# Optimization experiments

Measured on AMD Instinct MI355X. Metric: run time of the kernel, lower is better.

Reference implementation:

```python
import jax, jax.numpy as jnp
import numpy as np

N, E, F_IN, H, H2, G, C = 30000, 480000, 1280, 512, 256, 64, 10


def _linear_init(key, fan_in, fan_out):
    k1, k2 = jax.random.split(key)
    s = 1.0 / np.sqrt(fan_in)
    W = jax.random.uniform(k1, (fan_in, fan_out), jnp.float32, -s, s)
    b = jax.random.uniform(k2, (fan_out,), jnp.float32, -s, s)
    return W, b


def setup_inputs() -> dict:
    key = jax.random.key(0)
    ks = jax.random.split(key, 6)
    x = jax.random.normal(ks[0], (N, F_IN), jnp.float32)
    edge_index = jax.random.randint(ks[1], (2, E), 0, N, dtype=jnp.int32).astype(jnp.int64)
    batch = jnp.sort(jax.random.randint(ks[2], (N,), 0, G, dtype=jnp.int32)).astype(jnp.int64)
    W1, b1 = _linear_init(ks[3], F_IN, H)
    beta2 = jnp.ones((), jnp.float32)  # AGNNConv beta init = 1.0 (trainable in prop2)
    W2, b2 = _linear_init(ks[4], H, H2)
    W3, b3 = _linear_init(ks[5], 2 * H2, C)
    return {"x": x, "edge_index": edge_index, "batch": batch,
            "W1": W1, "b1": b1, "beta2": beta2,
            "W2": W2, "b2": b2, "W3": W3, "b3": b3}


def _agnn(x, src, dst, beta, n):
    # L2 normalize (PyG F.normalize: clamp norm at 1e-12)
    norm = jnp.maximum(jnp.linalg.norm(x, axis=-1, keepdims=True), 1e-12)
    xn = x / norm
    # per-edge cosine similarity attention logits
    alpha = beta * jnp.sum(xn[src] * xn[dst], axis=-1)  # [E']
    # softmax over incoming edges of each destination node
    amax = jax.ops.segment_max(alpha, dst, num_segments=n)
    ex = jnp.exp(alpha - amax[dst])
    denom = jax.ops.segment_sum(ex, dst, num_segments=n)
    w = ex / denom[dst]
    # weighted scatter-add of raw source features
    return jax.ops.segment_sum(w[:, None] * x[src], dst, num_segments=n)


def reference(x, edge_index, batch, W1, b1, beta2, W2, b2, W3, b3):
    n = x.shape[0]
    h = jax.nn.relu(x @ W1 + b1)  # [N, 512]
    # AGNNConv adds self-loops by default
    loops = jnp.arange(n, dtype=edge_index.dtype)
    src = jnp.concatenate([edge_index[0], loops])
    dst = jnp.concatenate([edge_index[1], loops])
    h = _agnn(h, src, dst, jnp.float32(1.0), n)  # prop1: fixed beta=1
    h = _agnn(h, src, dst, beta2, n)             # prop2: learned beta
    h = jax.nn.relu(h @ W2 + b2)  # [N, 256]
    # global max / mean pool per graph
    gmx = jax.ops.segment_max(h, batch, num_segments=G)
    cnt = jnp.maximum(jax.ops.segment_sum(jnp.ones((n,), h.dtype), batch, num_segments=G), 1.0)
    gav = jax.ops.segment_sum(h, batch, num_segments=G) / cnt[:, None]
    return jnp.concatenate([gmx, gav], axis=1) @ W3 + b3  # [G, C]
```

## Files before the change

### kernel.cpp

```cpp
#include <hip/hip_runtime.h>
#include <hip/hip_bf16.h>
#include <cstdint>


typedef __attribute__((ext_vector_type(8))) short bf16x8;
typedef __attribute__((ext_vector_type(4))) float f32x4;
typedef __attribute__((ext_vector_type(8))) unsigned short ushort8;
typedef __attribute__((ext_vector_type(4))) unsigned short ushort4v;
typedef __attribute__((ext_vector_type(4))) unsigned int uint4v;

__device__ inline unsigned short f2bf(float f) {
    unsigned int u = __float_as_uint(f);
    u += 0x7FFFu + ((u >> 16) & 1u);
    return (unsigned short)(u >> 16);
}

__device__ __forceinline__ float bf2f(unsigned short u) {
    return __uint_as_float(((unsigned int)u) << 16);
}

__device__ __forceinline__ unsigned int cvtpk(float lo, float hi) {
    unsigned int r;
    asm("v_cvt_pk_bf16_f32 %0, %1, %2" : "=v"(r) : "v"(lo), "v"(hi));
    return r;
}

__device__ __forceinline__ void gload_lds16(const void* g, void* l) {
    __builtin_amdgcn_global_load_lds(
        (const __attribute__((address_space(1))) void*)g,
        (__attribute__((address_space(3))) void*)l, 16, 0, 0);
}

__device__ __forceinline__ float wave_sum_dpp(float p) {
    int t;
    t = __builtin_amdgcn_update_dpp(0, __float_as_int(p), 0xB1, 0xf, 0xf, true);
    p += __int_as_float(t);
    t = __builtin_amdgcn_update_dpp(0, __float_as_int(p), 0x4E, 0xf, 0xf, true);
    p += __int_as_float(t);
    t = __builtin_amdgcn_update_dpp(0, __float_as_int(p), 0x141, 0xf, 0xf, true);
    p += __int_as_float(t);
    t = __builtin_amdgcn_update_dpp(0, __float_as_int(p), 0x140, 0xf, 0xf, true);
    p += __int_as_float(t);
    t = __builtin_amdgcn_update_dpp(0, __float_as_int(p), 0x142, 0xf, 0xf, true);
    p += __int_as_float(t);
    t = __builtin_amdgcn_update_dpp(0, __float_as_int(p), 0x143, 0xf, 0xf, true);
    p += __int_as_float(t);
    return __int_as_float(__builtin_amdgcn_readlane(__float_as_int(p), 63));
}

__device__ __forceinline__ float row16_sum_dpp(float p) {
    int t;
    t = __builtin_amdgcn_update_dpp(0, __float_as_int(p), 0xB1, 0xf, 0xf, true);
    p += __int_as_float(t);
    t = __builtin_amdgcn_update_dpp(0, __float_as_int(p), 0x4E, 0xf, 0xf, true);
    p += __int_as_float(t);
    t = __builtin_amdgcn_update_dpp(0, __float_as_int(p), 0x141, 0xf, 0xf, true);
    p += __int_as_float(t);
    t = __builtin_amdgcn_update_dpp(0, __float_as_int(p), 0x140, 0xf, 0xf, true);
    p += __int_as_float(t);
    return p;
}

__global__ __launch_bounds__(256) void k_transpose_both(
    const float* __restrict__ W1, unsigned short* __restrict__ W1T,
    int K1, int N1, int nt1,
    const float* __restrict__ W2, unsigned short* __restrict__ W2T,
    int K2, int N2) {
    __shared__ unsigned short tb[32][33];
    int id = blockIdx.x;
    const float* W; unsigned short* Wt; int K, N, bx, by;
    if (id < nt1) {
        W = W1; Wt = W1T; K = K1; N = N1;
        int nx = K1 / 32; bx = id % nx; by = id / nx;
    } else {
        id -= nt1;
        W = W2; Wt = W2T; K = K2; N = N2;
        int nx = K2 / 32; bx = id % nx; by = id / nx;
    }
    int k0 = bx * 32, n0 = by * 32;
    int tr = threadIdx.x >> 3;
    int tc = (threadIdx.x & 7) * 4;
    float4 v = *(const float4*)(W + (long)(k0 + tr) * N + n0 + tc);
    tb[tr][tc + 0] = f2bf(v.x); tb[tr][tc + 1] = f2bf(v.y);
    tb[tr][tc + 2] = f2bf(v.z); tb[tr][tc + 3] = f2bf(v.w);
    __syncthreads();
    ushort4v o = { tb[tc + 0][tr], tb[tc + 1][tr], tb[tc + 2][tr], tb[tc + 3][tr] };
    *(ushort4v*)(Wt + (long)(n0 + tr) * K + k0 + tc) = o;
}

template <int K, int BN, int NOUT, bool AF32, bool OUTBF16, bool PSUM_EN>
__global__ __launch_bounds__(512, 4) void k_gemm_bias_relu(
    const void* __restrict__ Av, const unsigned short* __restrict__ Bt,
    const float* __restrict__ bias, void* __restrict__ Cv,
    float* __restrict__ psum, int M) {
    constexpr int NSTEP = K / 32;
    constexpr int NF = BN / 64;
    constexpr int SLOTS = (NOUT / BN) * 4;
    __shared__ unsigned short As[2][128 * 32];
    __shared__ unsigned short Bs[2][BN * 32];
    int tid = threadIdx.x;
    int w = tid >> 6, l = tid & 63;
    int wm = w >> 2, wn = w & 3;
    int mBase = blockIdx.x * 128;
    int nBase = blockIdx.y * BN;

    const float* Af = (const float*)Av;
    const unsigned short* Ab = (const unsigned short*)Av;

    int arow = tid >> 2;
    int aslot = (tid & 3) ^ ((arow >> 1) & 3);
    long aRowG = mBase + arow; if (aRowG >= M) aRowG = M - 1;
    const float* aptr = AF32 ? (Af + aRowG * K + (tid & 3) * 8) : nullptr;

    auto stageB = [&](int b, int k0) {
#pragma unroll
        for (int o = 0; o < (BN + 127) / 128; ++o) {
            int rbase = (w * ((BN + 127) / 128) + o) * 16;
            int row = rbase + (l >> 2);
            int gsrc = (l & 3) ^ ((row >> 1) & 3);
            gload_lds16(Bt + (long)(nBase + row) * K + k0 + gsrc * 8,
                        &Bs[b][rbase * 32]);
        }
    };
    auto stageAbf = [&](int b, int k0) {
        int rbase = w * 16;
        int row = rbase + (l >> 2);
        int gsrc = (l & 3) ^ ((row >> 1) & 3);
        long gr = mBase + row; if (gr >= M) gr = M - 1;
        gload_lds16(Ab + gr * K + k0 + gsrc * 8, &As[b][rbase * 32]);
    };

    f32x4 acc[4][NF] = {};

    stageB(0, 0);
    if constexpr (AF32) {
        float4 z0 = *(const float4*)(aptr);
        float4 z1 = *(const float4*)(aptr + 4);
        uint4v p = { cvtpk(z0.x, z0.y), cvtpk(z0.z, z0.w),
                     cvtpk(z1.x, z1.y), cvtpk(z1.z, z1.w) };
        *(uint4v*)(&As[0][arow * 32 + aslot * 8]) = p;
    } else {
        stageAbf(0, 0);
    }
    __syncthreads();

    int s = 0;
    for (int step = 0; step < NSTEP; ++step, s ^= 1) {
        int nk = (step + 1) * 32;
        float4 f0, f1;
        if (nk < K) {
            stageB(s ^ 1, nk);
            if constexpr (AF32) {
                f0 = *(const float4*)(aptr + nk);
                f1 = *(const float4*)(aptr + nk + 4);
            } else {
                stageAbf(s ^ 1, nk);
            }
        }
        bf16x8 af[4];
#pragma unroll
        for (int m = 0; m < 4; ++m) {
            int ra = wm * 64 + m * 16 + (l & 15);
            int g = (l >> 4) ^ ((ra >> 1) & 3);
            af[m] = *(const bf16x8*)(&As[s][ra * 32 + g * 8]);
        }
#pragma unroll
        for (int n = 0; n < NF; ++n) {
            int rb = wn * (BN / 4) + n * 16 + (l & 15);
            int g = (l >> 4) ^ ((rb >> 1) & 3);
            bf16x8 bfr = *(const bf16x8*)(&Bs[s][rb * 32 + g * 8]);
#pragma unroll
            for (int m = 0; m < 4; ++m)
                acc[m][n] = __builtin_amdgcn_mfma_f32_16x16x32_bf16(
                    af[m], bfr, acc[m][n], 0, 0, 0);
        }
        if constexpr (AF32) {
            if (nk < K) {
                uint4v p = { cvtpk(f0.x, f0.y), cvtpk(f0.z, f0.w),
                             cvtpk(f1.x, f1.y), cvtpk(f1.z, f1.w) };
                *(uint4v*)(&As[s ^ 1][arow * 32 + aslot * 8]) = p;
            }
        }
        __syncthreads();
    }

    float bv[NF];
#pragma unroll
    for (int n = 0; n < NF; ++n)
        bv[n] = bias[nBase + wn * (BN / 4) + n * 16 + (l & 15)];
#pragma unroll
    for (int m = 0; m < 4; ++m) {
#pragma unroll
        for (int r = 0; r < 4; ++r) {
            int row = mBase + wm * 64 + m * 16 + (l >> 4) * 4 + r;
            float sq = 0.f;
#pragma unroll
            for (int n = 0; n < NF; ++n) {
                float v = fmaxf(acc[m][n][r] + bv[n], 0.f);
                sq += v * v;
                if (row < M) {
                    int colg = nBase + wn * (BN / 4) + n * 16 + (l & 15);
                    if constexpr (OUTBF16)
                        ((unsigned short*)Cv)[(long)row * NOUT + colg] = f2bf(v);
                    else
                        ((float*)Cv)[(long)row * NOUT + colg] = v;
                }
            }
            if constexpr (PSUM_EN) {
                sq = row16_sum_dpp(sq);
                if ((l & 15) == 0 && row < M)
                    psum[(long)row * SLOTS + blockIdx.y * 4 + wn] = sq;
            }
        }
    }
}

template <int SLOTS>
__global__ void k_rsqrt(const float* __restrict__ psum,
                        float* __restrict__ invn, int n) {
    int i = blockIdx.x * 256 + threadIdx.x;
    if (i >= n) return;
    const float* p = psum + (long)i * SLOTS;
    float s = 0.f;
#pragma unroll
    for (int j = 0; j < SLOTS; j += 4) {
        float4 a = *(const float4*)(p + j);
        s += (a.x + a.y) + (a.z + a.w);
    }
    invn[i] = 1.f / fmaxf(sqrtf(s), 1e-12f);
}

__global__ void k_csr_count(const int* __restrict__ ei, int* __restrict__ cnt, int E) {
    int e = blockIdx.x * blockDim.x + threadIdx.x;
    if (e < E) atomicAdd(&cnt[ei[E + e]], 1);
}

__global__ __launch_bounds__(1024) void k_scan1(const int* __restrict__ cnt,
                                                int* __restrict__ rowp,
                                                int* __restrict__ bsum, int n) {
    __shared__ int wsum[16];
    int b = blockIdx.x, t = threadIdx.x, lane = t & 63, w = t >> 6;
    int i = b * 1024 + t;
    int v = (i < n) ? cnt[i] + 1 : 0;
    int x = v;
#pragma unroll
    for (int off = 1; off < 64; off <<= 1) {
        int y = __shfl_up(x, off, 64);
        if (lane >= off) x += y;
    }
    if (lane == 63) wsum[w] = x;
    __syncthreads();
    if (t < 16) {
        int s = wsum[t];
#pragma unroll
        for (int off = 1; off < 16; off <<= 1) {
            int y = __shfl_up(s, off, 64);
            if (t >= off) s += y;
        }
        wsum[t] = s;
    }
    __syncthreads();
    int wo = w ? wsum[w - 1] : 0;
    if (i < n) rowp[i] = wo + x - v;
    if (t == 0) bsum[b] = wsum[15];
}

__global__ __launch_bounds__(1024) void k_scan23(const int* __restrict__ bsum,
                                                 int* __restrict__ rowp, int n, int nb) {
    __shared__ int off[65];
    int t = threadIdx.x;
    if (t < 64) {
        int v = (t < nb) ? bsum[t] : 0;
        int x = v;
#pragma unroll
        for (int o = 1; o < 64; o <<= 1) {
            int y = __shfl_up(x, o, 64);
            if (t >= o) x += y;
        }
        off[t] = x - v;
        if (t == nb - 1) off[64] = x;
    }
    __syncthreads();
    int i = blockIdx.x * 1024 + t;
    if (i < n) rowp[i] += off[i >> 10];
    else if (i == n) rowp[n] = off[64];
}

__global__ void k_csr_fill(const int* __restrict__ ei, const int* __restrict__ rowp,
                           int* __restrict__ fill, int* __restrict__ col, int E, int n) {
    int idx = blockIdx.x * blockDim.x + threadIdx.x;
    if (idx < E) {
        int d = ei[E + idx];
        int s = ei[idx];
        int pos = atomicAdd(&fill[d], 1);
        col[rowp[d] + pos] = s;
    } else if (idx < E + n) {
        int nd = idx - E;
        int pos = atomicAdd(&fill[nd], 1);
        col[rowp[nd] + pos] = nd;
    }
}

__global__ __launch_bounds__(256) void k_agnn(
    const unsigned short* __restrict__ h, const float* __restrict__ invn,
    const int* __restrict__ rowp, const int* __restrict__ col,
    const float* __restrict__ beta_ptr, unsigned short* __restrict__ out,
    float* __restrict__ invn_out, int nNodes) {
    int dst = blockIdx.x * 4 + (threadIdx.x >> 6);
    int lane = threadIdx.x & 63;
    if (dst >= nNodes) return;
    float beta = beta_ptr ? beta_ptr[0] : 1.0f;
    ushort8 hdv = *(const ushort8*)(h + (long)dst * 512 + lane * 8);
    float hd[8];
#pragma unroll
    for (int e = 0; e < 8; ++e) hd[e] = bf2f(hdv[e]);
    float coef = beta * invn[dst];
    float mshift = fabsf(beta) * 1.0625f;
    int s0 = rowp[dst], s1 = rowp[dst + 1];

    float ssum = 0.f;
    float accE[8] = {0.f, 0.f, 0.f, 0.f, 0.f, 0.f, 0.f, 0.f};
    float accO[8] = {0.f, 0.f, 0.f, 0.f, 0.f, 0.f, 0.f, 0.f};

    for (int base = s0; base < s1; base += 64) {
        int cnt = min(s1 - base, 64);
        int gi = base + lane; if (gi >= s1) gi = s1 - 1;
        int idxl = col[gi];
        float vinl = invn[idxl];
        ushort8 r0 = {}, r1 = {}, r2 = {}, r3 = {};
        r0 = *(const ushort8*)(h + (long)__builtin_amdgcn_readlane(idxl, 0) * 512 + lane * 8);
        if (cnt > 1) r1 = *(const ushort8*)(h + (long)__builtin_amdgcn_readlane(idxl, 1) * 512 + lane * 8);
        if (cnt > 2) r2 = *(const ushort8*)(h + (long)__builtin_amdgcn_readlane(idxl, 2) * 512 + lane * 8);
        if (cnt > 3) r3 = *(const ushort8*)(h + (long)__builtin_amdgcn_readlane(idxl, 3) * 512 + lane * 8);
        int j = 0;
        for (; j + 1 < cnt; j += 2) {
            ushort8 c0 = r0, c1 = r1;
            r0 = r2; r1 = r3;
            if (j + 4 < cnt) r2 = *(const ushort8*)(h + (long)__builtin_amdgcn_readlane(idxl, j + 4) * 512 + lane * 8);
            if (j + 5 < cnt) r3 = *(const ushort8*)(h + (long)__builtin_amdgcn_readlane(idxl, j + 5) * 512 + lane * 8);
            float a0[8], a1[8];
#pragma unroll
            for (int e = 0; e < 8; ++e) { a0[e] = bf2f(c0[e]); a1[e] = bf2f(c1[e]); }
            float p0 = a0[0] * hd[0] + a0[1] * hd[1] + a0[2] * hd[2] + a0[3] * hd[3] +
                       a0[4] * hd[4] + a0[5] * hd[5] + a0[6] * hd[6] + a0[7] * hd[7];
            float p1 = a1[0] * hd[0] + a1[1] * hd[1] + a1[2] * hd[2] + a1[3] * hd[3] +
                       a1[4] * hd[4] + a1[5] * hd[5] + a1[6] * hd[6] + a1[7] * hd[7];
            p0 = wave_sum_dpp(p0);
            p1 = wave_sum_dpp(p1);
            float al0 = coef * __int_as_float(__builtin_amdgcn_readlane(__float_as_int(vinl), j)) * p0;
            float al1 = coef * __int_as_float(__builtin_amdgcn_readlane(__float_as_int(vinl), j + 1)) * p1;
            float w0 = __expf(al0 - mshift);
            float w1 = __expf(al1 - mshift);
            ssum += w0 + w1;
#pragma unroll
            for (int e = 0; e < 8; ++e) { accE[e] += w0 * a0[e]; accO[e] += w1 * a1[e]; }
        }
        if (j < cnt) {
            float a0[8];
#pragma unroll
            for (int e = 0; e < 8; ++e) a0[e] = bf2f(r0[e]);
            float p0 = a0[0] * hd[0] + a0[1] * hd[1] + a0[2] * hd[2] + a0[3] * hd[3] +
                       a0[4] * hd[4] + a0[5] * hd[5] + a0[6] * hd[6] + a0[7] * hd[7];
            p0 = wave_sum_dpp(p0);
            float al0 = coef * __int_as_float(__builtin_amdgcn_readlane(__float_as_int(vinl), j)) * p0;
            float w0 = __expf(al0 - mshift);
            ssum += w0;
#pragma unroll
            for (int e = 0; e < 8; ++e) accE[e] += w0 * a0[e];
        }
    }
    float inv_s = 1.f / ssum;
    float acc[8];
#pragma unroll
    for (int e = 0; e < 8; ++e) acc[e] = (accE[e] + accO[e]) * inv_s;

    uint4v o = { cvtpk(acc[0], acc[1]), cvtpk(acc[2], acc[3]),
                 cvtpk(acc[4], acc[5]), cvtpk(acc[6], acc[7]) };
    *(uint4v*)(out + (long)dst * 512 + lane * 8) = o;

    if (invn_out) {
        float s = 0.f;
#pragma unroll
        for (int e = 0; e < 8; ++e) s += acc[e] * acc[e];
        s = wave_sum_dpp(s);
        if (lane == 0) invn_out[dst] = 1.f / fmaxf(sqrtf(s), 1e-12f);
    }
}

__global__ __launch_bounds__(256) void k_pool_final(
    const unsigned short* __restrict__ h3, const int* __restrict__ batch,
    const float* __restrict__ W3, const float* __restrict__ b3,
    float* __restrict__ out, int n, int C) {
    __shared__ int se[2];
    __shared__ float wpart[4];
    int g = blockIdx.x;
    int t = threadIdx.x;
    if (t < 2) {
        int tgt = g + t;
        int lo = 0, hi = n;
        while (lo < hi) {
            int mid = (lo + hi) >> 1;
            if (batch[mid] < tgt) lo = mid + 1; else hi = mid;
        }
        se[t] = lo;
    }
    __syncthreads();
    int s = se[0], e = se[1];
    float mx = -3.402823466e38f, sm = 0.f;
    int r = s;
    for (; r + 4 <= e; r += 4) {
        float v0 = bf2f(h3[(long)(r + 0) * 256 + t]);
        float v1 = bf2f(h3[(long)(r + 1) * 256 + t]);
        float v2 = bf2f(h3[(long)(r + 2) * 256 + t]);
        float v3 = bf2f(h3[(long)(r + 3) * 256 + t]);
        mx = fmaxf(mx, fmaxf(fmaxf(v0, v1), fmaxf(v2, v3)));
        sm += (v0 + v1) + (v2 + v3);
    }
    for (; r < e; ++r) {
        float v = bf2f(h3[(long)r * 256 + t]);
        mx = fmaxf(mx, v); sm += v;
    }
    float cnt = fmaxf((float)(e - s), 1.f);
    float av = sm / cnt;
    for (int c = 0; c < C; ++c) {
        float part = mx * W3[(long)t * C + c] + av * W3[(long)(256 + t) * C + c];
        part = wave_sum_dpp(part);
        if ((t & 63) == 0) wpart[t >> 6] = part;
        __syncthreads();
        if (t == 0)
            out[g * C + c] = wpart[0] + wpart[1] + wpart[2] + wpart[3] + b3[c];
        __syncthreads();
    }
}

extern "C" void kernel_launch(void* const* d_in, const int* in_sizes, int n_in,
                              void* d_out, int out_size, void* d_ws, size_t ws_size,
                              hipStream_t stream) {
    const float* x     = (const float*)d_in[0];
    const int*   ei    = (const int*)d_in[1];
    const int*   batch = (const int*)d_in[2];
    const float* W1    = (const float*)d_in[3];
    const float* b1    = (const float*)d_in[4];
    const float* beta2 = (const float*)d_in[5];
    const float* W2    = (const float*)d_in[6];
    const float* b2    = (const float*)d_in[7];
    const float* W3    = (const float*)d_in[8];
    const float* b3    = (const float*)d_in[9];
    float* out = (float*)d_out;

    const int N = in_sizes[2];
    const int E = in_sizes[1] / 2;
    const int F_IN = in_sizes[0] / N;
    const int H = in_sizes[4];
    const int H2 = in_sizes[7];
    const int C = in_sizes[9];
    const int G = out_size / C;

    char* ws = (char*)d_ws;
    unsigned short* H1B = (unsigned short*)(ws + 0);
    unsigned short* H3B = (unsigned short*)(ws + 0);
    unsigned short* HPB = (unsigned short*)(ws + 31000000L);
    unsigned short* H2B = (unsigned short*)(ws + 62000000L);
    unsigned short* W1T = (unsigned short*)(ws + 93000000L);
    unsigned short* W2T = (unsigned short*)(ws + 94500000L);
    float* INVN_A = (float*)(ws + 95000000L);
    float* INVN_B = (float*)(ws + 95200000L);
    int*   CNT    = (int*)(ws + 95400000L);
    int*   FILL   = (int*)(ws + 95600000L);
    int*   ROWP   = (int*)(ws + 95800000L);
    int*   COL    = (int*)(ws + 96000000L);
    int*   BSUM   = (int*)(ws + 98100000L);
    float* PSUM   = (float*)(ws + 98110000L);

    hipMemsetAsync(ws + 95400000L, 0, 400000, stream);

    int nt1 = (F_IN / 32) * (H / 32);
    int nt2 = (H / 32) * (H2 / 32);
    k_transpose_both<<<nt1 + nt2, 256, 0, stream>>>(W1, W1T, F_IN, H, nt1,
                                                    W2, W2T, H, H2);

    int nb = (N + 1023) / 1024;
    k_csr_count<<<(E + 255) / 256, 256, 0, stream>>>(ei, CNT, E);
    k_scan1<<<nb, 1024, 0, stream>>>(CNT, ROWP, BSUM, N);
    k_scan23<<<(N + 1 + 1023) / 1024, 1024, 0, stream>>>(BSUM, ROWP, N, nb);
    k_csr_fill<<<(E + N + 255) / 256, 256, 0, stream>>>(ei, ROWP, FILL, COL, E, N);

    {
        dim3 grid((N + 127) / 128, H / 256);
        k_gemm_bias_relu<1280, 256, 512, true, true, true>
            <<<grid, 512, 0, stream>>>(x, W1T, b1, H1B, PSUM, N);
    }
    k_rsqrt<8><<<(N + 255) / 256, 256, 0, stream>>>(PSUM, INVN_A, N);

    k_agnn<<<(N + 3) / 4, 256, 0, stream>>>(H1B, INVN_A, ROWP, COL, nullptr, HPB, INVN_B, N);

    k_agnn<<<(N + 3) / 4, 256, 0, stream>>>(HPB, INVN_B, ROWP, COL, beta2, H2B, nullptr, N);

    {
        dim3 grid((N + 127) / 128, H2 / 128);
        k_gemm_bias_relu<512, 128, 256, false, true, false>
            <<<grid, 512, 0, stream>>>(H2B, W2T, b2, H3B, nullptr, N);
    }

    k_pool_final<<<G, 256, 0, stream>>>(H3B, batch, W3, b3, out, N, C);
}
```

Before: 342.2 us.

## Swizzle GEMM blocks across XCDs and narrow the first GEMM's N tile

Both bias+ReLU GEMMs now use a 1D grid with a remapped block index. The N-tiles that share the same 128-row M tile are placed on the same XCD (block index mod 8), so the A rows they all read can be reused from that XCD's L2 instead of being fetched again from HBM. The first GEMM also drops its N tile from 256 to 128, giving four N-blocks and twice as many workgroups. To match, the per-row partial-norm buffer grows to 16 slots and the rsqrt kernel reads 16 slots. The risk is that the large fp32 input is now read by four blocks per M tile instead of two, so any L2 misses cost more traffic. The narrower tile also lowers MFMA work per loaded A element.

```diff
diff --git a/kernel.cpp b/kernel.cpp
--- a/kernel.cpp
+++ b/kernel.cpp
@@ -88,7 +88,7 @@
     *(ushort4v*)(Wt + (long)(n0 + tr) * K + k0 + tc) = o;
 }
 
-template <int K, int BN, int NOUT, bool AF32, bool OUTBF16, bool PSUM_EN>
+template <int K, int BN, int NOUT, int NNB, bool AF32, bool OUTBF16, bool PSUM_EN>
 __global__ __launch_bounds__(512, 4) void k_gemm_bias_relu(
     const void* __restrict__ Av, const unsigned short* __restrict__ Bt,
     const float* __restrict__ bias, void* __restrict__ Cv,
@@ -101,8 +101,14 @@
     int tid = threadIdx.x;
     int w = tid >> 6, l = tid & 63;
     int wm = w >> 2, wn = w & 3;
-    int mBase = blockIdx.x * 128;
-    int nBase = blockIdx.y * BN;
+
+    int b = blockIdx.x;
+    int xcd = b & 7, loc = b >> 3;
+    int nIdx = loc % NNB;
+    int mIdx = (loc / NNB) * 8 + xcd;
+    if (mIdx * 128 >= M) return;
+    int mBase = mIdx * 128;
+    int nBase = nIdx * BN;
 
     const float* Af = (const float*)Av;
     const unsigned short* Ab = (const unsigned short*)Av;
@@ -112,22 +118,22 @@
     long aRowG = mBase + arow; if (aRowG >= M) aRowG = M - 1;
     const float* aptr = AF32 ? (Af + aRowG * K + (tid & 3) * 8) : nullptr;
 
-    auto stageB = [&](int b, int k0) {
+    auto stageB = [&](int bb, int k0) {
 #pragma unroll
         for (int o = 0; o < (BN + 127) / 128; ++o) {
             int rbase = (w * ((BN + 127) / 128) + o) * 16;
             int row = rbase + (l >> 2);
             int gsrc = (l & 3) ^ ((row >> 1) & 3);
             gload_lds16(Bt + (long)(nBase + row) * K + k0 + gsrc * 8,
-                        &Bs[b][rbase * 32]);
+                        &Bs[bb][rbase * 32]);
         }
     };
-    auto stageAbf = [&](int b, int k0) {
+    auto stageAbf = [&](int bb, int k0) {
         int rbase = w * 16;
         int row = rbase + (l >> 2);
         int gsrc = (l & 3) ^ ((row >> 1) & 3);
         long gr = mBase + row; if (gr >= M) gr = M - 1;
-        gload_lds16(Ab + gr * K + k0 + gsrc * 8, &As[b][rbase * 32]);
+        gload_lds16(Ab + gr * K + k0 + gsrc * 8, &As[bb][rbase * 32]);
     };
 
     f32x4 acc[4][NF] = {};
@@ -209,7 +215,7 @@
             if constexpr (PSUM_EN) {
                 sq = row16_sum_dpp(sq);
                 if ((l & 15) == 0 && row < M)
-                    psum[(long)row * SLOTS + blockIdx.y * 4 + wn] = sq;
+                    psum[(long)row * SLOTS + nIdx * 4 + wn] = sq;
             }
         }
     }
@@ -485,22 +491,19 @@
     k_scan23<<<(N + 1 + 1023) / 1024, 1024, 0, stream>>>(BSUM, ROWP, N, nb);
     k_csr_fill<<<(E + N + 255) / 256, 256, 0, stream>>>(ei, ROWP, FILL, COL, E, N);
 
-    {
-        dim3 grid((N + 127) / 128, H / 256);
-        k_gemm_bias_relu<1280, 256, 512, true, true, true>
-            <<<grid, 512, 0, stream>>>(x, W1T, b1, H1B, PSUM, N);
-    }
-    k_rsqrt<8><<<(N + 255) / 256, 256, 0, stream>>>(PSUM, INVN_A, N);
+    int nmt = (N + 127) / 128;
+    int nmt8 = ((nmt + 7) / 8) * 8;
+
+    k_gemm_bias_relu<1280, 128, 512, 4, true, true, true>
+        <<<nmt8 * 4, 512, 0, stream>>>(x, W1T, b1, H1B, PSUM, N);
+    k_rsqrt<16><<<(N + 255) / 256, 256, 0, stream>>>(PSUM, INVN_A, N);
 
     k_agnn<<<(N + 3) / 4, 256, 0, stream>>>(H1B, INVN_A, ROWP, COL, nullptr, HPB, INVN_B, N);
 
     k_agnn<<<(N + 3) / 4, 256, 0, stream>>>(HPB, INVN_B, ROWP, COL, beta2, H2B, nullptr, N);
 
-    {
-        dim3 grid((N + 127) / 128, H2 / 128);
-        k_gemm_bias_relu<512, 128, 256, false, true, false>
-            <<<grid, 512, 0, stream>>>(H2B, W2T, b2, H3B, nullptr, N);
-    }
+    k_gemm_bias_relu<512, 128, 256, 2, false, true, false>
+        <<<nmt8 * 2, 512, 0, stream>>>(H2B, W2T, b2, H3B, nullptr, N);
 
     k_pool_final<<<G, 256, 0, stream>>>(H3B, batch, W3, b3, out, N, C);
 }
```

Measured after the change: 356.0 us. 4.0% more time.
